# Optimization experiments

Hardware: AMD Instinct MI355X
Metric: run time of the kernel (lower is better)

The kernel has to match this reference:

```python
import jax, jax.numpy as jnp
import numpy as np
import math

HIDDEN = 128; NHEADS = 4; N_COE = 50; N_SCALES = 4; THRE = 5.0; S = 4096; B = 1


def setup_inputs():
    key = jax.random.key(0)
    ks = jax.random.split(key, 12)
    w = lambda k, shape: jax.random.normal(k, shape, jnp.float32) * 0.05
    return {
        "eigenvalue": jax.random.uniform(ks[0], (B, S), jnp.float32) * 2.0,  # graph Laplacian eigvals in [0,2)
        "length": jnp.full((B,), S, dtype=jnp.int32),
        "sele_num": jnp.full((B,), S, dtype=jnp.int32),
        "eig_w_W": w(ks[1], (HIDDEN + 1, HIDDEN)), "eig_w_b": jnp.zeros((HIDDEN,), jnp.float32),
        "mha_ln_g": jnp.ones((HIDDEN,), jnp.float32), "mha_ln_b": jnp.zeros((HIDDEN,), jnp.float32),
        "in_W": w(ks[2], (HIDDEN, 3 * HIDDEN)), "in_b": jnp.zeros((3 * HIDDEN,), jnp.float32),
        "out_W": w(ks[3], (HIDDEN, HIDDEN)), "out_b": jnp.zeros((HIDDEN,), jnp.float32),
        "ffn_ln_g": jnp.ones((HIDDEN,), jnp.float32), "ffn_ln_b": jnp.zeros((HIDDEN,), jnp.float32),
        "ffn1_W": w(ks[4], (HIDDEN, HIDDEN)), "ffn1_b": jnp.zeros((HIDDEN,), jnp.float32),
        "ffn2_W": w(ks[5], (HIDDEN, HIDDEN)), "ffn2_b": jnp.zeros((HIDDEN,), jnp.float32),
        "dsc_W": w(ks[6], (HIDDEN, N_COE)), "dsc_b": jnp.zeros((N_COE,), jnp.float32),
        "dwv_W": w(ks[7], (HIDDEN, N_COE)), "dwv_b": jnp.zeros((N_COE,), jnp.float32),
        "dss_W": w(ks[8], (HIDDEN, N_SCALES)), "dss_b": jnp.zeros((N_SCALES,), jnp.float32),
    }


def layer_norm(x, g, b, eps=1e-5):
    m = x.mean(-1, keepdims=True)
    v = ((x - m) ** 2).mean(-1, keepdims=True)
    return (x - m) / jnp.sqrt(v + eps) * g + b


def sine_encoding(e, W, b):
    # e: [B, S] -> [B, S, HIDDEN]
    div = jnp.exp(jnp.arange(0, HIDDEN, 2, dtype=e.dtype) * (-math.log(10000.0) / HIDDEN))
    pe = (e * 100.0)[..., None] * div  # [B, S, HIDDEN/2]
    eeig = jnp.concatenate([e[..., None], jnp.sin(pe), jnp.cos(pe)], axis=-1)  # [B, S, HIDDEN+1]
    return eeig @ W + b


def mha(x, pad_mask, in_W, in_b, out_W, out_b):
    # x: [B, S, D]; pad_mask: [B, S] True = masked key
    Bb, Ss, D = x.shape
    hd = D // NHEADS
    qkv = x @ in_W + in_b
    q, k, v = jnp.split(qkv, 3, axis=-1)
    hsplit = lambda t: t.reshape(Bb, Ss, NHEADS, hd).transpose(0, 2, 1, 3)  # [B, H, S, hd]
    q, k, v = hsplit(q), hsplit(k), hsplit(v)
    scores = jnp.einsum('bhqd,bhkd->bhqk', q, k) / math.sqrt(hd)
    scores = jnp.where(pad_mask[:, None, None, :], -jnp.inf, scores)
    attn = jax.nn.softmax(scores, axis=-1)
    o = jnp.einsum('bhqk,bhkd->bhqd', attn, v).transpose(0, 2, 1, 3).reshape(Bb, Ss, D)
    return o @ out_W + out_b


def cheb_base(y, n_coe, flag):
    # Chebyshev recurrence: wavelet = [T_0, T_2, ...], scaling = [T_1, T_3, ...]
    te0 = jnp.ones_like(y)
    to0 = y
    def step(carry, _):
        te, to = carry
        te = 2.0 * y * to - te
        to = 2.0 * y * te - to
        return (te, to), (te, to)
    _, (evens, odds) = jax.lax.scan(step, (te0, to0), None, length=n_coe - 1)
    if flag == 'scaling':
        base = jnp.concatenate([to0[None], odds], axis=0)   # [n_coe, B, S, d]
    else:
        base = jnp.concatenate([te0[None], evens], axis=0)
    return jnp.moveaxis(base, 0, 1)  # [B, n_coe, S, d]


def _forward(eigenvalue, eig_w_W, eig_w_b, mha_ln_g, mha_ln_b, in_W, in_b, out_W, out_b,
             ffn_ln_g, ffn_ln_b, ffn1_W, ffn1_b, ffn2_W, ffn2_b,
             dsc_W, dsc_b, dwv_W, dwv_b, dss_W, dss_b, length, sele_num):
    Bb, Ss = eigenvalue.shape
    eve = eigenvalue
    eig_mask = jnp.arange(Ss)[None, :] >= sele_num[:, None]  # [B, S] True = pad
    # --- EigenEncoding (dropout in eval mode = identity) ---
    eig = sine_encoding(eve, eig_w_W, eig_w_b)
    eig = eig + mha(layer_norm(eig, mha_ln_g, mha_ln_b), eig_mask, in_W, in_b, out_W, out_b)
    f = layer_norm(eig, ffn_ln_g, ffn_ln_b)
    f = jax.nn.gelu(f @ ffn1_W + ffn1_b, approximate=False) @ ffn2_W + ffn2_b
    eig_filter = eig + f  # [B, S, HIDDEN]
    lenf = length.astype(eve.dtype)[:, None]
    def pooled(W, b):
        c = eig_filter @ W + b
        c = jnp.where(eig_mask[..., None], 0.0, c)
        return c.sum(axis=1) / (lenf + 1e-8)
    coe_scaling = jax.nn.sigmoid(pooled(dsc_W, dsc_b))
    coe_scaling = coe_scaling / (coe_scaling.sum(-1, keepdims=True) + 1e-8)  # [B, n_coe]
    coe_wavelet = jax.nn.sigmoid(pooled(dwv_W, dwv_b))
    coe_wavelet = coe_wavelet / (coe_wavelet.sum(-1, keepdims=True) + 1e-8)
    coe_scales = jax.nn.sigmoid(pooled(dss_W, dss_b)) * THRE  # [B, n_scales]
    # --- Chebyshev bases ---
    base_scaling = cheb_base(eve[..., None] - 1.0, N_COE, 'scaling')  # [B, n_coe, S, 1]
    fsw = eve[..., None] * coe_scales[:, None, :]                      # [B, S, n_scales]
    fsw = jnp.where(fsw > 2.0, 0.0, fsw)
    base_wavelet = cheb_base(fsw - 1.0, N_COE, 'wavelet')             # [B, n_coe, S, n_scales]
    base_scaling = 0.5 * (1.0 - base_scaling)
    base_wavelet = 0.5 * (1.0 - base_wavelet)
    curr_scaling = jnp.einsum('bc,bcsd->bsd', coe_scaling, base_scaling)
    curr_wavelet = jnp.einsum('bc,bcsd->bsd', coe_wavelet, base_wavelet)
    out = jnp.concatenate([curr_scaling, curr_wavelet], axis=-1)       # [B, S, 1+n_scales]
    out = out / (jnp.linalg.norm(out, axis=-1, keepdims=True) + 1e-8)  # cfg.lam.tight_use = True
    return out


def reference(eigenvalue, length, sele_num, eig_w_W, eig_w_b, mha_ln_g, mha_ln_b, in_W, in_b,
              out_W, out_b, ffn_ln_g, ffn_ln_b, ffn1_W, ffn1_b, ffn2_W, ffn2_b,
              dsc_W, dsc_b, dwv_W, dwv_b, dss_W, dss_b):
    return _forward(eigenvalue, eig_w_W, eig_w_b, mha_ln_g, mha_ln_b, in_W, in_b, out_W, out_b,
                    ffn_ln_g, ffn_ln_b, ffn1_W, ffn1_b, ffn2_W, ffn2_b,
                    dsc_W, dsc_b, dwv_W, dwv_b, dss_W, dss_b, length, sele_num)
```

## Files before the change

### kernel.cpp

```cpp
#include <hip/hip_runtime.h>
#include <math.h>


#define KSPLIT 4

typedef __attribute__((ext_vector_type(8))) short short8;
typedef __attribute__((ext_vector_type(4))) short short4v;
typedef __attribute__((ext_vector_type(4))) float f32x4;

__device__ inline unsigned short f2bf(float x) {
    unsigned u = __float_as_uint(x);
    return (unsigned short)((u + 0x7FFFu + ((u >> 16) & 1u)) >> 16);
}
__device__ inline float bf2f(unsigned short h) { return __uint_as_float(((unsigned)h) << 16); }

__global__ __launch_bounds__(256) void k_embed(const float* __restrict__ eve,
    const float* __restrict__ eigW, const float* __restrict__ ebias,
    const float* __restrict__ g, const float* __restrict__ b,
    const float* __restrict__ inW, const float* __restrict__ inb,
    float* __restrict__ eig, float* __restrict__ qkv, unsigned short* __restrict__ Khi_g,
    unsigned short* __restrict__ Klo_g, unsigned short* __restrict__ Vt_g)
{
    __shared__ __align__(16) float wsh[129 * 128];
    __shared__ __align__(16) float se[16][132];
    __shared__ __align__(16) float xn[16][132];
    __shared__ __align__(16) unsigned short vsh[128][16];
    const int t = threadIdx.x;
    const int r0 = blockIdx.x * 16;
    {
        const int r = t >> 4, l4 = t & 15;
        const float e = eve[r0 + r];
        if (l4 == 0) se[r][128] = e;
        #pragma unroll
        for (int jj = 0; jj < 4; ++jj) {
            const int j = l4 * 4 + jj;
            const float div = __expf(-0.07195578415606394f * (float)(2 * j));
            const float pe = e * 100.0f * div;
            se[r][j]      = __sinf(pe);
            se[r][64 + j] = __cosf(pe);
        }
    }
    {
        const float4* __restrict__ src = (const float4*)eigW;
        float4* dst = (float4*)wsh;
        #pragma unroll
        for (int i = 0; i < 17; ++i) {
            const int f = t + i * 256;
            if (f < 4128) dst[f] = src[f];
        }
    }
    __syncthreads();
    const int lane = t & 63;
    const int w = t >> 6;
    const int rp = w * 2 + (lane >> 5);
    const int c0 = (lane & 31) * 4;
    const int ra = rp * 2, rb = ra + 1;
    float xa[4], xb[4];
    {
        const float4 w0 = *(const float4*)&wsh[c0];
        const float ea = se[ra][128], eb = se[rb][128];
        float a0 = ea * w0.x, a1 = ea * w0.y, a2 = ea * w0.z, a3 = ea * w0.w;
        float b0 = eb * w0.x, b1 = eb * w0.y, b2 = eb * w0.z, b3 = eb * w0.w;
        #pragma unroll 8
        for (int k = 0; k < 128; ++k) {
            const float xva = se[ra][k];
            const float xvb = se[rb][k];
            const float4 wk = *(const float4*)&wsh[(k + 1) * 128 + c0];
            a0 = fmaf(xva, wk.x, a0); a1 = fmaf(xva, wk.y, a1);
            a2 = fmaf(xva, wk.z, a2); a3 = fmaf(xva, wk.w, a3);
            b0 = fmaf(xvb, wk.x, b0); b1 = fmaf(xvb, wk.y, b1);
            b2 = fmaf(xvb, wk.z, b2); b3 = fmaf(xvb, wk.w, b3);
        }
        const float4 bb = *(const float4*)&ebias[c0];
        xa[0] = a0 + bb.x; xa[1] = a1 + bb.y; xa[2] = a2 + bb.z; xa[3] = a3 + bb.w;
        xb[0] = b0 + bb.x; xb[1] = b1 + bb.y; xb[2] = b2 + bb.z; xb[3] = b3 + bb.w;
        *(float4*)&eig[(size_t)(r0 + ra) * 128 + c0] = make_float4(xa[0], xa[1], xa[2], xa[3]);
        *(float4*)&eig[(size_t)(r0 + rb) * 128 + c0] = make_float4(xb[0], xb[1], xb[2], xb[3]);
    }
    {
        float sa = (xa[0] + xa[1]) + (xa[2] + xa[3]);
        float qa = (xa[0] * xa[0] + xa[1] * xa[1]) + (xa[2] * xa[2] + xa[3] * xa[3]);
        float sb = (xb[0] + xb[1]) + (xb[2] + xb[3]);
        float qb = (xb[0] * xb[0] + xb[1] * xb[1]) + (xb[2] * xb[2] + xb[3] * xb[3]);
        #pragma unroll
        for (int m = 1; m < 32; m <<= 1) {
            sa += __shfl_xor(sa, m, 32); qa += __shfl_xor(qa, m, 32);
            sb += __shfl_xor(sb, m, 32); qb += __shfl_xor(qb, m, 32);
        }
        const float ma = sa * (1.f / 128.f), mb = sb * (1.f / 128.f);
        const float ia = 1.f / sqrtf(qa * (1.f / 128.f) - ma * ma + 1e-5f);
        const float ib = 1.f / sqrtf(qb * (1.f / 128.f) - mb * mb + 1e-5f);
        const float4 gg = *(const float4*)&g[c0];
        const float4 bb = *(const float4*)&b[c0];
        *(float4*)&xn[ra][c0] = make_float4((xa[0] - ma) * ia * gg.x + bb.x,
                                            (xa[1] - ma) * ia * gg.y + bb.y,
                                            (xa[2] - ma) * ia * gg.z + bb.z,
                                            (xa[3] - ma) * ia * gg.w + bb.w);
        *(float4*)&xn[rb][c0] = make_float4((xb[0] - mb) * ib * gg.x + bb.x,
                                            (xb[1] - mb) * ib * gg.y + bb.y,
                                            (xb[2] - mb) * ib * gg.z + bb.z,
                                            (xb[3] - mb) * ib * gg.w + bb.w);
    }
    const int rowa = r0 + ra, rowb = r0 + rb;
    for (int p = 0; p < 3; ++p) {
        __syncthreads();
        {
            const float4* __restrict__ src = (const float4*)inW;
            float4* dst = (float4*)wsh;
            #pragma unroll
            for (int i = 0; i < 16; ++i) {
                const int f = t + i * 256;
                const int k = f >> 5, c4 = f & 31;
                dst[f] = src[k * 96 + p * 32 + c4];
            }
        }
        __syncthreads();
        float A[4], B[4];
        {
            const float4 bb = *(const float4*)&inb[p * 128 + c0];
            A[0] = bb.x; A[1] = bb.y; A[2] = bb.z; A[3] = bb.w;
            B[0] = bb.x; B[1] = bb.y; B[2] = bb.z; B[3] = bb.w;
        }
        #pragma unroll 8
        for (int k = 0; k < 128; ++k) {
            const float xva = xn[ra][k];
            const float xvb = xn[rb][k];
            const float4 wk = *(const float4*)&wsh[k * 128 + c0];
            A[0] = fmaf(xva, wk.x, A[0]); A[1] = fmaf(xva, wk.y, A[1]);
            A[2] = fmaf(xva, wk.z, A[2]); A[3] = fmaf(xva, wk.w, A[3]);
            B[0] = fmaf(xvb, wk.x, B[0]); B[1] = fmaf(xvb, wk.y, B[1]);
            B[2] = fmaf(xvb, wk.z, B[2]); B[3] = fmaf(xvb, wk.w, B[3]);
        }
        if (p == 0) {
            *(float4*)&qkv[(size_t)rowa * 384 + c0] = make_float4(A[0], A[1], A[2], A[3]);
            *(float4*)&qkv[(size_t)rowb * 384 + c0] = make_float4(B[0], B[1], B[2], B[3]);
        } else if (p == 1) {
            const int h = c0 >> 5, d = c0 & 31;
            unsigned short h4[4], l4v[4];
            #pragma unroll
            for (int i = 0; i < 4; ++i) { h4[i] = f2bf(A[i]); l4v[i] = f2bf(A[i] - bf2f(h4[i])); }
            *(uint2*)&Khi_g[((size_t)h * 4096 + rowa) * 32 + d] = *(uint2*)h4;
            *(uint2*)&Klo_g[((size_t)h * 4096 + rowa) * 32 + d] = *(uint2*)l4v;
            #pragma unroll
            for (int i = 0; i < 4; ++i) { h4[i] = f2bf(B[i]); l4v[i] = f2bf(B[i] - bf2f(h4[i])); }
            *(uint2*)&Khi_g[((size_t)h * 4096 + rowb) * 32 + d] = *(uint2*)h4;
            *(uint2*)&Klo_g[((size_t)h * 4096 + rowb) * 32 + d] = *(uint2*)l4v;
        } else {
            #pragma unroll
            for (int i = 0; i < 4; ++i) {
                vsh[c0 + i][ra] = f2bf(A[i]);
                vsh[c0 + i][rb] = f2bf(B[i]);
            }
        }
    }
    __syncthreads();
    if (t < 128) {
        const uint4 v0 = *(const uint4*)&vsh[t][0];
        const uint4 v1 = *(const uint4*)&vsh[t][8];
        *(uint4*)&Vt_g[(size_t)t * 4096 + r0]     = v0;
        *(uint4*)&Vt_g[(size_t)t * 4096 + r0 + 8] = v1;
    }
}

#define KSTR 40
#define VSTR 72
#define PSTR 72

__global__ __launch_bounds__(256) void k_attn(const float* __restrict__ qkv,
    const unsigned short* __restrict__ Khi_g, const unsigned short* __restrict__ Klo_g,
    const unsigned short* __restrict__ Vt_g,
    const int* __restrict__ sele, float* __restrict__ Oe, float* __restrict__ E)
{
    __shared__ __align__(16) unsigned short Khi[64 * KSTR];
    __shared__ __align__(16) unsigned short Klo[64 * KSTR];
    __shared__ __align__(16) unsigned short Vt[32 * VSTR];
    __shared__ __align__(16) unsigned short Pb[4][16 * PSTR];

    const int t = threadIdx.x;
    const int lane = t & 63;
    const int l = lane & 15;
    const int quad = lane >> 4;
    const int wv = __builtin_amdgcn_readfirstlane(t >> 6);
    const int qb = blockIdx.x;
    const int h  = blockIdx.y;
    const int ks = blockIdx.z;
    const int nk = sele[0];

    short8 qhi, qlo;
    {
        const float* __restrict__ qr = qkv + (size_t)(qb * 64 + wv * 16 + l) * 384 + h * 32 + quad * 8;
        const float4 a = *(const float4*)qr;
        const float4 b = *(const float4*)(qr + 4);
        const float sc = 0.17677669529663687f;
        float v[8] = {a.x * sc, a.y * sc, a.z * sc, a.w * sc, b.x * sc, b.y * sc, b.z * sc, b.w * sc};
        #pragma unroll
        for (int j = 0; j < 8; ++j) {
            const unsigned short hb = f2bf(v[j]);
            qhi[j] = (short)hb;
            qlo[j] = (short)f2bf(v[j] - bf2f(hb));
        }
    }
    f32x4 accO0 = {0.f, 0.f, 0.f, 0.f};
    f32x4 accO1 = {0.f, 0.f, 0.f, 0.f};
    float elane = 0.f;

    const int kk = t >> 2;
    const int d0 = (t & 3) * 8;
    const int vd = t >> 3;
    const int ko = (t & 7) * 8;

    for (int ch = 0; ch < 16; ++ch) {
        const int keybase = ks * 1024 + ch * 64;
        __syncthreads();
        {
            const uint4 kh16 = *(const uint4*)&Khi_g[((size_t)h * 4096 + keybase + kk) * 32 + d0];
            const uint4 kl16 = *(const uint4*)&Klo_g[((size_t)h * 4096 + keybase + kk) * 32 + d0];
            const uint4 vv16 = *(const uint4*)&Vt_g[((size_t)h * 32 + vd) * 4096 + keybase + ko];
            *(uint4*)&Khi[kk * KSTR + d0] = kh16;
            *(uint4*)&Klo[kk * KSTR + d0] = kl16;
            *(uint4*)&Vt[vd * VSTR + ko]  = vv16;
        }
        __syncthreads();
        unsigned short* __restrict__ Pw = Pb[wv];
        #pragma unroll
        for (int tile = 0; tile < 4; ++tile) {
            const int kl = tile * 16 + l;
            const short8 kh = *(const short8*)&Khi[kl * KSTR + quad * 8];
            const short8 kw = *(const short8*)&Klo[kl * KSTR + quad * 8];
            f32x4 S = {0.f, 0.f, 0.f, 0.f};
            S = __builtin_amdgcn_mfma_f32_16x16x32_bf16(kh, qhi, S, 0, 0, 0);
            S = __builtin_amdgcn_mfma_f32_16x16x32_bf16(kw, qhi, S, 0, 0, 0);
            S = __builtin_amdgcn_mfma_f32_16x16x32_bf16(kh, qlo, S, 0, 0, 0);
            const int kg0 = keybase + tile * 16 + quad * 4;
            short4v pw;
            #pragma unroll
            for (int r = 0; r < 4; ++r) {
                const float p = (kg0 + r < nk) ? __expf(S[r]) : 0.f;
                elane += p;
                pw[r] = (short)f2bf(p);
            }
            *(short4v*)&Pw[l * PSTR + tile * 16 + quad * 4] = pw;
        }
        #pragma unroll
        for (int step = 0; step < 2; ++step) {
            const short8 pa  = *(const short8*)&Pw[l * PSTR + step * 32 + quad * 8];
            const short8 vb0 = *(const short8*)&Vt[l * VSTR + step * 32 + quad * 8];
            const short8 vb1 = *(const short8*)&Vt[(16 + l) * VSTR + step * 32 + quad * 8];
            accO0 = __builtin_amdgcn_mfma_f32_16x16x32_bf16(pa, vb0, accO0, 0, 0, 0);
            accO1 = __builtin_amdgcn_mfma_f32_16x16x32_bf16(pa, vb1, accO1, 0, 0, 0);
        }
    }
    elane += __shfl_xor(elane, 16, 64);
    elane += __shfl_xor(elane, 32, 64);
    const int qrow0 = qb * 64 + wv * 16;
    if (lane < 16)
        E[((size_t)ks * 4 + h) * 4096 + qrow0 + l] = elane;
    #pragma unroll
    for (int r = 0; r < 4; ++r) {
        const size_t row = qrow0 + quad * 4 + r;
        Oe[((size_t)ks * 4096 + row) * 128 + h * 32 + l]      = accO0[r];
        Oe[((size_t)ks * 4096 + row) * 128 + h * 32 + 16 + l] = accO1[r];
    }
}

__global__ __launch_bounds__(256) void k_ffn(const float* __restrict__ eig,
    const float* __restrict__ Oe, const float* __restrict__ E,
    const float* __restrict__ outW, const float* __restrict__ outb,
    const float* __restrict__ lg, const float* __restrict__ lb,
    const float* __restrict__ W1, const float* __restrict__ b1,
    const float* __restrict__ W2, const float* __restrict__ b2,
    const int* __restrict__ sele, float* __restrict__ xsum)
{
    __shared__ __align__(16) float wsh[128 * 128];
    __shared__ __align__(16) float sA[16][132];
    __shared__ __align__(16) float xn[16][132];
    __shared__ __align__(16) float cs[16][132];
    const int t = threadIdx.x;
    const int r0 = blockIdx.x * 16;
    {
        const int r = t >> 4, c8 = (t & 15) * 8;
        const int h = c8 >> 5;
        float es = 0.f;
        float v[8] = {0.f, 0.f, 0.f, 0.f, 0.f, 0.f, 0.f, 0.f};
        #pragma unroll
        for (int ks = 0; ks < KSPLIT; ++ks) {
            es += E[((size_t)ks * 4 + h) * 4096 + r0 + r];
            const float4 o1 = *(const float4*)&Oe[((size_t)ks * 4096 + r0 + r) * 128 + c8];
            const float4 o2 = *(const float4*)&Oe[((size_t)ks * 4096 + r0 + r) * 128 + c8 + 4];
            v[0] += o1.x; v[1] += o1.y; v[2] += o1.z; v[3] += o1.w;
            v[4] += o2.x; v[5] += o2.y; v[6] += o2.z; v[7] += o2.w;
        }
        const float rcp = 1.f / es;
        *(float4*)&sA[r][c8]     = make_float4(v[0] * rcp, v[1] * rcp, v[2] * rcp, v[3] * rcp);
        *(float4*)&sA[r][c8 + 4] = make_float4(v[4] * rcp, v[5] * rcp, v[6] * rcp, v[7] * rcp);
    }
    {
        const float4* __restrict__ src = (const float4*)outW;
        float4* dst = (float4*)wsh;
        #pragma unroll
        for (int i = 0; i < 16; ++i) dst[t + i * 256] = src[t + i * 256];
    }
    __syncthreads();
    const int lane = t & 63;
    const int w = t >> 6;
    const int rp = w * 2 + (lane >> 5);
    const int c0 = (lane & 31) * 4;
    const int ra = rp * 2, rb = ra + 1;
    float x2a[4], x2b[4];
    {
        const float4 bb = *(const float4*)&outb[c0];
        float a0 = bb.x, a1 = bb.y, a2 = bb.z, a3 = bb.w;
        float b0 = bb.x, b1 = bb.y, b2 = bb.z, b3 = bb.w;
        #pragma unroll 8
        for (int k = 0; k < 128; ++k) {
            const float xva = sA[ra][k];
            const float xvb = sA[rb][k];
            const float4 wk = *(const float4*)&wsh[k * 128 + c0];
            a0 = fmaf(xva, wk.x, a0); a1 = fmaf(xva, wk.y, a1);
            a2 = fmaf(xva, wk.z, a2); a3 = fmaf(xva, wk.w, a3);
            b0 = fmaf(xvb, wk.x, b0); b1 = fmaf(xvb, wk.y, b1);
            b2 = fmaf(xvb, wk.z, b2); b3 = fmaf(xvb, wk.w, b3);
        }
        const float4 ea = *(const float4*)&eig[(size_t)(r0 + ra) * 128 + c0];
        const float4 eb = *(const float4*)&eig[(size_t)(r0 + rb) * 128 + c0];
        x2a[0] = ea.x + a0; x2a[1] = ea.y + a1; x2a[2] = ea.z + a2; x2a[3] = ea.w + a3;
        x2b[0] = eb.x + b0; x2b[1] = eb.y + b1; x2b[2] = eb.z + b2; x2b[3] = eb.w + b3;
    }
    {
        float sa = (x2a[0] + x2a[1]) + (x2a[2] + x2a[3]);
        float qa = (x2a[0] * x2a[0] + x2a[1] * x2a[1]) + (x2a[2] * x2a[2] + x2a[3] * x2a[3]);
        float sb = (x2b[0] + x2b[1]) + (x2b[2] + x2b[3]);
        float qb = (x2b[0] * x2b[0] + x2b[1] * x2b[1]) + (x2b[2] * x2b[2] + x2b[3] * x2b[3]);
        #pragma unroll
        for (int m = 1; m < 32; m <<= 1) {
            sa += __shfl_xor(sa, m, 32); qa += __shfl_xor(qa, m, 32);
            sb += __shfl_xor(sb, m, 32); qb += __shfl_xor(qb, m, 32);
        }
        const float ma = sa * (1.f / 128.f), mb = sb * (1.f / 128.f);
        const float ia = 1.f / sqrtf(qa * (1.f / 128.f) - ma * ma + 1e-5f);
        const float ib = 1.f / sqrtf(qb * (1.f / 128.f) - mb * mb + 1e-5f);
        const float4 gg = *(const float4*)&lg[c0];
        const float4 bb = *(const float4*)&lb[c0];
        *(float4*)&xn[ra][c0] = make_float4((x2a[0] - ma) * ia * gg.x + bb.x,
                                            (x2a[1] - ma) * ia * gg.y + bb.y,
                                            (x2a[2] - ma) * ia * gg.z + bb.z,
                                            (x2a[3] - ma) * ia * gg.w + bb.w);
        *(float4*)&xn[rb][c0] = make_float4((x2b[0] - mb) * ib * gg.x + bb.x,
                                            (x2b[1] - mb) * ib * gg.y + bb.y,
                                            (x2b[2] - mb) * ib * gg.z + bb.z,
                                            (x2b[3] - mb) * ib * gg.w + bb.w);
    }
    __syncthreads();
    {
        const float4* __restrict__ src = (const float4*)W1;
        float4* dst = (float4*)wsh;
        #pragma unroll
        for (int i = 0; i < 16; ++i) dst[t + i * 256] = src[t + i * 256];
    }
    __syncthreads();
    {
        const float4 bb = *(const float4*)&b1[c0];
        float a0 = bb.x, a1 = bb.y, a2 = bb.z, a3 = bb.w;
        float b0 = bb.x, b1v = bb.y, b2v = bb.z, b3 = bb.w;
        #pragma unroll 8
        for (int k = 0; k < 128; ++k) {
            const float xva = xn[ra][k];
            const float xvb = xn[rb][k];
            const float4 wk = *(const float4*)&wsh[k * 128 + c0];
            a0 = fmaf(xva, wk.x, a0); a1 = fmaf(xva, wk.y, a1);
            a2 = fmaf(xva, wk.z, a2); a3 = fmaf(xva, wk.w, a3);
            b0 = fmaf(xvb, wk.x, b0); b1v = fmaf(xvb, wk.y, b1v);
            b2v = fmaf(xvb, wk.z, b2v); b3 = fmaf(xvb, wk.w, b3);
        }
        *(float4*)&sA[ra][c0] = make_float4(
            0.5f * a0 * (1.f + erff(a0 * 0.70710678118654752f)),
            0.5f * a1 * (1.f + erff(a1 * 0.70710678118654752f)),
            0.5f * a2 * (1.f + erff(a2 * 0.70710678118654752f)),
            0.5f * a3 * (1.f + erff(a3 * 0.70710678118654752f)));
        *(float4*)&sA[rb][c0] = make_float4(
            0.5f * b0 * (1.f + erff(b0 * 0.70710678118654752f)),
            0.5f * b1v * (1.f + erff(b1v * 0.70710678118654752f)),
            0.5f * b2v * (1.f + erff(b2v * 0.70710678118654752f)),
            0.5f * b3 * (1.f + erff(b3 * 0.70710678118654752f)));
    }
    __syncthreads();
    {
        const float4* __restrict__ src = (const float4*)W2;
        float4* dst = (float4*)wsh;
        #pragma unroll
        for (int i = 0; i < 16; ++i) dst[t + i * 256] = src[t + i * 256];
    }
    __syncthreads();
    {
        const float4 bb = *(const float4*)&b2[c0];
        float a0 = bb.x, a1 = bb.y, a2 = bb.z, a3 = bb.w;
        float b0 = bb.x, b1v = bb.y, b2v = bb.z, b3 = bb.w;
        #pragma unroll 8
        for (int k = 0; k < 128; ++k) {
            const float xva = sA[ra][k];
            const float xvb = sA[rb][k];
            const float4 wk = *(const float4*)&wsh[k * 128 + c0];
            a0 = fmaf(xva, wk.x, a0); a1 = fmaf(xva, wk.y, a1);
            a2 = fmaf(xva, wk.z, a2); a3 = fmaf(xva, wk.w, a3);
            b0 = fmaf(xvb, wk.x, b0); b1v = fmaf(xvb, wk.y, b1v);
            b2v = fmaf(xvb, wk.z, b2v); b3 = fmaf(xvb, wk.w, b3);
        }
        const int nsel = sele[0];
        const bool ina = (r0 + ra) < nsel, inb2 = (r0 + rb) < nsel;
        *(float4*)&cs[ra][c0] = ina ? make_float4(x2a[0] + a0, x2a[1] + a1, x2a[2] + a2, x2a[3] + a3)
                                    : make_float4(0.f, 0.f, 0.f, 0.f);
        *(float4*)&cs[rb][c0] = inb2 ? make_float4(x2b[0] + b0, x2b[1] + b1v, x2b[2] + b2v, x2b[3] + b3)
                                     : make_float4(0.f, 0.f, 0.f, 0.f);
    }
    __syncthreads();
    if (t < 128) {
        float s = 0.f;
        #pragma unroll
        for (int rr = 0; rr < 16; ++rr) s += cs[rr][t];
        atomicAdd(&xsum[t], s);
    }
}

__global__ __launch_bounds__(512) void k_coef(const float* __restrict__ xsum,
    const float* __restrict__ dscW, const float* __restrict__ dscb,
    const float* __restrict__ dwvW, const float* __restrict__ dwvb,
    const float* __restrict__ dssW, const float* __restrict__ dssb,
    const int* __restrict__ len, const int* __restrict__ sele,
    float* __restrict__ coef)
{
    __shared__ float xs[128];
    __shared__ float part[104][4];
    __shared__ float val[104];
    __shared__ float s2[2];
    const int t = threadIdx.x;
    if (t < 128) xs[t] = xsum[t];
    __syncthreads();
    const float invl = 1.f / ((float)len[0] + 1e-8f);
    const float ns = (float)sele[0];
    const int o = t >> 2, lk = t & 3;
    if (o < 104) {
        const float* Wp; int stride, col;
        if (o < 50)       { Wp = dscW; stride = 50; col = o; }
        else if (o < 100) { Wp = dwvW; stride = 50; col = o - 50; }
        else              { Wp = dssW; stride = 4;  col = o - 100; }
        float a = 0.f;
        #pragma unroll
        for (int kk = 0; kk < 32; ++kk) {
            const int k = lk * 32 + kk;
            a = fmaf(xs[k], Wp[k * stride + col], a);
        }
        part[o][lk] = a;
    }
    __syncthreads();
    if (t < 104) {
        const float bias = (t < 50) ? dscb[t] : ((t < 100) ? dwvb[t - 50] : dssb[t - 100]);
        float a = ((part[t][0] + part[t][1]) + (part[t][2] + part[t][3]) + ns * bias) * invl;
        val[t] = 1.f / (1.f + __expf(-a));
    }
    __syncthreads();
    if (t == 0) { float s = 0.f; for (int i = 0; i < 50; ++i) s += val[i]; s2[0] = s; }
    if (t == 1) { float s = 0.f; for (int i = 0; i < 50; ++i) s += val[50 + i]; s2[1] = s; }
    __syncthreads();
    if (t < 50) {
        coef[t]      = val[t] / (s2[0] + 1e-8f);
        coef[50 + t] = val[50 + t] / (s2[1] + 1e-8f);
    } else if (t >= 100 && t < 104) {
        coef[t] = val[t] * 5.0f;
    }
}

__global__ __launch_bounds__(128) void k_out(const float* __restrict__ eve,
    const float* __restrict__ coef, float* __restrict__ out)
{
    __shared__ float csc[50], cwv[50], cssh[4];
    const int t = threadIdx.x;
    if (t < 50) csc[t] = coef[t];
    else if (t < 100) cwv[t - 50] = coef[t];
    else if (t < 104) cssh[t - 100] = coef[t];
    __syncthreads();
    const int s = blockIdx.x * 128 + t;
    const float e = eve[s];
    float vals[5];
    {
        const float y = e - 1.f;
        float te = 1.f, to = y;
        float a = csc[0] * (0.5f * (1.f - to));
        const float y2 = 2.f * y;
        for (int i = 1; i < 50; ++i) {
            te = fmaf(y2, to, -te);
            to = fmaf(y2, te, -to);
            a = fmaf(csc[i], 0.5f * (1.f - to), a);
        }
        vals[0] = a;
    }
    #pragma unroll
    for (int j = 0; j < 4; ++j) {
        float f = e * cssh[j];
        if (f > 2.f) f = 0.f;
        const float y = f - 1.f;
        float te = 1.f, to = y;
        float a = cwv[0] * (0.5f * (1.f - te));
        const float y2 = 2.f * y;
        for (int i = 1; i < 50; ++i) {
            te = fmaf(y2, to, -te);
            to = fmaf(y2, te, -to);
            a = fmaf(cwv[i], 0.5f * (1.f - te), a);
        }
        vals[1 + j] = a;
    }
    float n2 = 0.f;
    #pragma unroll
    for (int k = 0; k < 5; ++k) n2 += vals[k] * vals[k];
    const float invn = 1.f / (sqrtf(n2) + 1e-8f);
    #pragma unroll
    for (int k = 0; k < 5; ++k) out[s * 5 + k] = vals[k] * invn;
}

extern "C" void kernel_launch(void* const* d_in, const int* in_sizes, int n_in,
                              void* d_out, int out_size, void* d_ws, size_t ws_size,
                              hipStream_t stream) {
    const float* eve  = (const float*)d_in[0];
    const int*   len  = (const int*)d_in[1];
    const int*   sele = (const int*)d_in[2];
    const float* eigW = (const float*)d_in[3];
    const float* eigB = (const float*)d_in[4];
    const float* mlg  = (const float*)d_in[5];
    const float* mlb  = (const float*)d_in[6];
    const float* inW  = (const float*)d_in[7];
    const float* inb  = (const float*)d_in[8];
    const float* outW = (const float*)d_in[9];
    const float* outb = (const float*)d_in[10];
    const float* flg  = (const float*)d_in[11];
    const float* flb  = (const float*)d_in[12];
    const float* W1   = (const float*)d_in[13];
    const float* b1   = (const float*)d_in[14];
    const float* W2   = (const float*)d_in[15];
    const float* b2   = (const float*)d_in[16];
    const float* dscW = (const float*)d_in[17];
    const float* dscb = (const float*)d_in[18];
    const float* dwvW = (const float*)d_in[19];
    const float* dwvb = (const float*)d_in[20];
    const float* dssW = (const float*)d_in[21];
    const float* dssb = (const float*)d_in[22];

    float* ws   = (float*)d_ws;
    float* eig  = ws;
    float* qkv  = ws + 524288;
    float* Oe   = ws + 2097152;
    float* E    = ws + 4194304;
    float* xsum = ws + 4259840;
    float* coef = ws + 4259968;
    unsigned short* Khi_g = (unsigned short*)(ws + 4260352);
    unsigned short* Klo_g = (unsigned short*)(ws + 4522496);
    unsigned short* Vt_g  = (unsigned short*)(ws + 4784640);
    float* out  = (float*)d_out;

    hipMemsetAsync(xsum, 0, 128 * sizeof(float), stream);
    k_embed<<<256, 256, 0, stream>>>(eve, eigW, eigB, mlg, mlb, inW, inb,
                                     eig, qkv, Khi_g, Klo_g, Vt_g);
    k_attn <<<dim3(64, 4, KSPLIT), 256, 0, stream>>>(qkv, Khi_g, Klo_g, Vt_g, sele, Oe, E);
    k_ffn  <<<256, 256, 0, stream>>>(eig, Oe, E, outW, outb, flg, flb, W1, b1, W2, b2, sele, xsum);
    k_coef <<<1, 512, 0, stream>>>(xsum, dscW, dscb, dwvW, dwvb, dssW, dssb, len, sele, coef);
    k_out  <<<32, 128, 0, stream>>>(eve, coef, out);
}
```

Baseline: 187.6 us.

## Run attention blocks as single waves handling all four query fragments

The attention kernel moves from four 64-thread waves per block, each owning 16 query rows, to a single 64-thread wave that owns all 64 query rows of the block. The K/V chunk loads are spread across the one wave, and each K fragment loaded from LDS is reused across four query fragments. This removes the two per-chunk `__syncthreads` barriers and cuts LDS reads of K and V per query row. In exchange the kernel has four times fewer waves in flight, which leaves less latency hiding for the unprefetched global loads, and each wave holds more registers.

```diff
diff --git a/kernel.cpp b/kernel.cpp
--- a/kernel.cpp
+++ b/kernel.cpp
@@ -166,7 +166,7 @@
 #define VSTR 72
 #define PSTR 72
 
-__global__ __launch_bounds__(256) void k_attn(const float* __restrict__ qkv,
+__global__ __launch_bounds__(64) void k_attn(const float* __restrict__ qkv,
     const unsigned short* __restrict__ Khi_g, const unsigned short* __restrict__ Klo_g,
     const unsigned short* __restrict__ Vt_g,
     const int* __restrict__ sele, float* __restrict__ Oe, float* __restrict__ E)
@@ -174,21 +174,21 @@
     __shared__ __align__(16) unsigned short Khi[64 * KSTR];
     __shared__ __align__(16) unsigned short Klo[64 * KSTR];
     __shared__ __align__(16) unsigned short Vt[32 * VSTR];
-    __shared__ __align__(16) unsigned short Pb[4][16 * PSTR];
-
-    const int t = threadIdx.x;
-    const int lane = t & 63;
+    __shared__ __align__(16) unsigned short Pw[64 * PSTR];
+
+    const int lane = threadIdx.x;
     const int l = lane & 15;
     const int quad = lane >> 4;
-    const int wv = __builtin_amdgcn_readfirstlane(t >> 6);
     const int qb = blockIdx.x;
     const int h  = blockIdx.y;
     const int ks = blockIdx.z;
     const int nk = sele[0];
 
-    short8 qhi, qlo;
-    {
-        const float* __restrict__ qr = qkv + (size_t)(qb * 64 + wv * 16 + l) * 384 + h * 32 + quad * 8;
+    short8 qhi[4], qlo[4];
+    #pragma unroll
+    for (int qf = 0; qf < 4; ++qf) {
+        const float* __restrict__ qr =
+            qkv + (size_t)(qb * 64 + qf * 16 + l) * 384 + h * 32 + quad * 8;
         const float4 a = *(const float4*)qr;
         const float4 b = *(const float4*)(qr + 4);
         const float sc = 0.17677669529663687f;
@@ -196,70 +196,96 @@
         #pragma unroll
         for (int j = 0; j < 8; ++j) {
             const unsigned short hb = f2bf(v[j]);
-            qhi[j] = (short)hb;
-            qlo[j] = (short)f2bf(v[j] - bf2f(hb));
-        }
-    }
-    f32x4 accO0 = {0.f, 0.f, 0.f, 0.f};
-    f32x4 accO1 = {0.f, 0.f, 0.f, 0.f};
-    float elane = 0.f;
-
-    const int kk = t >> 2;
-    const int d0 = (t & 3) * 8;
-    const int vd = t >> 3;
-    const int ko = (t & 7) * 8;
+            qhi[qf][j] = (short)hb;
+            qlo[qf][j] = (short)f2bf(v[j] - bf2f(hb));
+        }
+    }
+    f32x4 accO[4][2];
+    #pragma unroll
+    for (int qf = 0; qf < 4; ++qf) {
+        accO[qf][0] = (f32x4){0.f, 0.f, 0.f, 0.f};
+        accO[qf][1] = (f32x4){0.f, 0.f, 0.f, 0.f};
+    }
+    float elane[4] = {0.f, 0.f, 0.f, 0.f};
 
     for (int ch = 0; ch < 16; ++ch) {
         const int keybase = ks * 1024 + ch * 64;
-        __syncthreads();
         {
-            const uint4 kh16 = *(const uint4*)&Khi_g[((size_t)h * 4096 + keybase + kk) * 32 + d0];
-            const uint4 kl16 = *(const uint4*)&Klo_g[((size_t)h * 4096 + keybase + kk) * 32 + d0];
-            const uint4 vv16 = *(const uint4*)&Vt_g[((size_t)h * 32 + vd) * 4096 + keybase + ko];
-            *(uint4*)&Khi[kk * KSTR + d0] = kh16;
-            *(uint4*)&Klo[kk * KSTR + d0] = kl16;
-            *(uint4*)&Vt[vd * VSTR + ko]  = vv16;
-        }
-        __syncthreads();
-        unsigned short* __restrict__ Pw = Pb[wv];
+            uint4 kh[4], kl4[4], vv[4];
+            #pragma unroll
+            for (int j = 0; j < 4; ++j) {
+                const int kk = (lane >> 2) + 16 * j;
+                const int o4 = (lane & 3) * 8;
+                kh[j]  = *(const uint4*)&Khi_g[((size_t)h * 4096 + keybase + kk) * 32 + o4];
+                kl4[j] = *(const uint4*)&Klo_g[((size_t)h * 4096 + keybase + kk) * 32 + o4];
+            }
+            #pragma unroll
+            for (int j = 0; j < 4; ++j) {
+                const int vd = (lane >> 3) + 8 * j;
+                const int ko = (lane & 7) * 8;
+                vv[j] = *(const uint4*)&Vt_g[((size_t)h * 32 + vd) * 4096 + keybase + ko];
+            }
+            #pragma unroll
+            for (int j = 0; j < 4; ++j) {
+                const int kk = (lane >> 2) + 16 * j;
+                const int o4 = (lane & 3) * 8;
+                *(uint4*)&Khi[kk * KSTR + o4] = kh[j];
+                *(uint4*)&Klo[kk * KSTR + o4] = kl4[j];
+            }
+            #pragma unroll
+            for (int j = 0; j < 4; ++j) {
+                const int vd = (lane >> 3) + 8 * j;
+                const int ko = (lane & 7) * 8;
+                *(uint4*)&Vt[vd * VSTR + ko] = vv[j];
+            }
+        }
         #pragma unroll
         for (int tile = 0; tile < 4; ++tile) {
             const int kl = tile * 16 + l;
             const short8 kh = *(const short8*)&Khi[kl * KSTR + quad * 8];
             const short8 kw = *(const short8*)&Klo[kl * KSTR + quad * 8];
-            f32x4 S = {0.f, 0.f, 0.f, 0.f};
-            S = __builtin_amdgcn_mfma_f32_16x16x32_bf16(kh, qhi, S, 0, 0, 0);
-            S = __builtin_amdgcn_mfma_f32_16x16x32_bf16(kw, qhi, S, 0, 0, 0);
-            S = __builtin_amdgcn_mfma_f32_16x16x32_bf16(kh, qlo, S, 0, 0, 0);
             const int kg0 = keybase + tile * 16 + quad * 4;
-            short4v pw;
-            #pragma unroll
-            for (int r = 0; r < 4; ++r) {
-                const float p = (kg0 + r < nk) ? __expf(S[r]) : 0.f;
-                elane += p;
-                pw[r] = (short)f2bf(p);
-            }
-            *(short4v*)&Pw[l * PSTR + tile * 16 + quad * 4] = pw;
+            #pragma unroll
+            for (int qf = 0; qf < 4; ++qf) {
+                f32x4 S = {0.f, 0.f, 0.f, 0.f};
+                S = __builtin_amdgcn_mfma_f32_16x16x32_bf16(kh, qhi[qf], S, 0, 0, 0);
+                S = __builtin_amdgcn_mfma_f32_16x16x32_bf16(kw, qhi[qf], S, 0, 0, 0);
+                S = __builtin_amdgcn_mfma_f32_16x16x32_bf16(kh, qlo[qf], S, 0, 0, 0);
+                short4v pw;
+                #pragma unroll
+                for (int r = 0; r < 4; ++r) {
+                    const float p = (kg0 + r < nk) ? __expf(S[r]) : 0.f;
+                    elane[qf] += p;
+                    pw[r] = (short)f2bf(p);
+                }
+                *(short4v*)&Pw[(qf * 16 + l) * PSTR + tile * 16 + quad * 4] = pw;
+            }
         }
         #pragma unroll
         for (int step = 0; step < 2; ++step) {
-            const short8 pa  = *(const short8*)&Pw[l * PSTR + step * 32 + quad * 8];
             const short8 vb0 = *(const short8*)&Vt[l * VSTR + step * 32 + quad * 8];
             const short8 vb1 = *(const short8*)&Vt[(16 + l) * VSTR + step * 32 + quad * 8];
-            accO0 = __builtin_amdgcn_mfma_f32_16x16x32_bf16(pa, vb0, accO0, 0, 0, 0);
-            accO1 = __builtin_amdgcn_mfma_f32_16x16x32_bf16(pa, vb1, accO1, 0, 0, 0);
-        }
-    }
-    elane += __shfl_xor(elane, 16, 64);
-    elane += __shfl_xor(elane, 32, 64);
-    const int qrow0 = qb * 64 + wv * 16;
-    if (lane < 16)
-        E[((size_t)ks * 4 + h) * 4096 + qrow0 + l] = elane;
+            #pragma unroll
+            for (int qf = 0; qf < 4; ++qf) {
+                const short8 pa = *(const short8*)&Pw[(qf * 16 + l) * PSTR + step * 32 + quad * 8];
+                accO[qf][0] = __builtin_amdgcn_mfma_f32_16x16x32_bf16(pa, vb0, accO[qf][0], 0, 0, 0);
+                accO[qf][1] = __builtin_amdgcn_mfma_f32_16x16x32_bf16(pa, vb1, accO[qf][1], 0, 0, 0);
+            }
+        }
+    }
     #pragma unroll
-    for (int r = 0; r < 4; ++r) {
-        const size_t row = qrow0 + quad * 4 + r;
-        Oe[((size_t)ks * 4096 + row) * 128 + h * 32 + l]      = accO0[r];
-        Oe[((size_t)ks * 4096 + row) * 128 + h * 32 + 16 + l] = accO1[r];
+    for (int qf = 0; qf < 4; ++qf) {
+        float e = elane[qf];
+        e += __shfl_xor(e, 16, 64);
+        e += __shfl_xor(e, 32, 64);
+        if (lane < 16)
+            E[((size_t)ks * 4 + h) * 4096 + qb * 64 + qf * 16 + l] = e;
+        #pragma unroll
+        for (int r = 0; r < 4; ++r) {
+            const size_t row = qb * 64 + qf * 16 + quad * 4 + r;
+            Oe[((size_t)ks * 4096 + row) * 128 + h * 32 + l]      = accO[qf][0][r];
+            Oe[((size_t)ks * 4096 + row) * 128 + h * 32 + 16 + l] = accO[qf][1][r];
+        }
     }
 }
 
@@ -558,7 +584,7 @@
     hipMemsetAsync(xsum, 0, 128 * sizeof(float), stream);
     k_embed<<<256, 256, 0, stream>>>(eve, eigW, eigB, mlg, mlb, inW, inb,
                                      eig, qkv, Khi_g, Klo_g, Vt_g);
-    k_attn <<<dim3(64, 4, KSPLIT), 256, 0, stream>>>(qkv, Khi_g, Klo_g, Vt_g, sele, Oe, E);
+    k_attn <<<dim3(64, 4, KSPLIT), 64, 0, stream>>>(qkv, Khi_g, Klo_g, Vt_g, sele, Oe, E);
     k_ffn  <<<256, 256, 0, stream>>>(eig, Oe, E, outW, outb, flg, flb, W1, b1, W2, b2, sele, xsum);
     k_coef <<<1, 512, 0, stream>>>(xsum, dscW, dscb, dwvW, dwvb, dssW, dssb, len, sele, coef);
     k_out  <<<32, 128, 0, stream>>>(eve, coef, out);
```

Measured after the change: 234.6 us. +25.0%, slower.
